# Performance work log

Measured on AMD Instinct MI355X. Metric: run time of the kernel, lower is better.

## Reference

```python
import jax, jax.numpy as jnp
import numpy as np

K = 10  # topk classes


def setup_inputs() -> dict:
    key = jax.random.key(0)
    ks = jax.random.split(key, 12)
    B, DF, M, C, V, DW, DT = 64, 768, 26, 3129, 10000, 300, 1024
    s = lambda k, sh, scale: jax.random.normal(k, sh, dtype=jnp.float32) * scale
    return {
        "ftm": s(ks[0], (B, DF, M, M), 1.0),
        "logits": s(ks[1], (B, C), 1.0),
        "labels": jax.random.randint(ks[2], (B,), 0, C, dtype=jnp.int32),
        "indices_table": jax.random.randint(ks[3], (C, 4), 0, V, dtype=jnp.int32),
        "word2vec": s(ks[4], (V, DW), 1.0),
        "W_emb": s(ks[5], (DW, DT), 1.0 / np.sqrt(DW)),
        "b_emb": jnp.zeros((DT,), jnp.float32),
        "W_cls": s(ks[6], (DT, DT), 1.0 / np.sqrt(DT)),
        "b_cls": jnp.zeros((DT,), jnp.float32),
        "W_v": s(ks[7], (DF, DT), 1.0 / np.sqrt(DF)),
        "b_v": jnp.zeros((DT,), jnp.float32),
        "W_bap": s(ks[8], (DT, DT), 1.0 / np.sqrt(DT)),
        "b_bap": jnp.zeros((DT,), jnp.float32),
        "W_fc": s(ks[9], (DT, K), 1.0 / np.sqrt(DT)),
        "b_fc": jnp.zeros((K,), jnp.float32),
    }


def reference(ftm, logits, labels, indices_table, word2vec,
              W_emb, b_emb, W_cls, b_cls, W_v, b_v, W_bap, b_bap, W_fc, b_fc):
    B, DF = ftm.shape[0], ftm.shape[1]
    C = logits.shape[1]
    # dispatch: topk classes, gather their word indices, embed
    _, topk_idx = jax.lax.top_k(logits, K)                  # [B, K]
    topk_cls = indices_table[topk_idx]                      # [B, K, 4]
    emb = word2vec[topk_cls].mean(axis=2)                   # [B, K, 300] (ClassEmbedding pooling)
    cls_emb = jax.nn.relu(emb @ W_emb + b_emb)              # [B, K, 1024]
    # SAC_BAP (dropouts in eval mode = identity)
    cls_emb = jax.nn.relu(cls_emb @ W_cls + b_cls)          # [B, K, 1024]
    f = ftm.reshape(B, DF, -1).transpose(0, 2, 1)           # [B, F, 768], F = m*m
    v = jax.nn.relu(f @ W_v + b_v)                          # [B, F, 1024]
    att_w_b_sfx = jnp.einsum('bfd,bkd->bfk', v, cls_emb)    # [B, F, K]
    att_w = jax.nn.softmax(att_w_b_sfx, axis=1)             # softmax over positions
    bap = jnp.einsum('bfd,bfk,bkd->bd', v, att_w, cls_emb)  # [B, 1024]
    bap = jax.nn.relu(bap @ W_bap + b_bap)                  # bap_emb_FC
    bap_logits = bap @ W_fc + b_fc                          # fc_new 1x1 conv -> [B, K]
    # combine: scatter topk logits into the full class space
    um = jnp.zeros((B, C), dtype=bap_logits.dtype)
    um = um.at[jnp.arange(B)[:, None], topk_idx].set(bap_logits)
    return um
```

## Files before the change

kernel.cpp:

```cpp
#include <hip/hip_runtime.h>
#include <hip/hip_bf16.h>

#define B_   64
#define C_   3129
#define K_   10
#define DF_  768
#define F_   676
#define DW_  300
#define DWP_ 320
#define DT_  1024
#define NSEG 4
#define FSEG 169

typedef __attribute__((ext_vector_type(8))) short short8;
typedef __attribute__((ext_vector_type(4))) float floatx4;

__device__ __forceinline__ void gload_lds16(const void* g, void* l) {
    __builtin_amdgcn_global_load_lds(
        (const __attribute__((address_space(1))) void*)g,
        (__attribute__((address_space(3))) void*)l, 16, 0, 0);
}

__global__ void topk_kernel(const float* __restrict__ logits,
                            int* __restrict__ topk_idx) {
    __shared__ float vals[C_];
    __shared__ float red_v[256];
    __shared__ int   red_i[256];
    int b = blockIdx.x;
    int tid = threadIdx.x;
    for (int i = tid; i < C_; i += 256) vals[i] = logits[(size_t)b * C_ + i];
    __syncthreads();
    for (int sel = 0; sel < K_; ++sel) {
        float bv = -INFINITY; int bi = 0x7fffffff;
        for (int i = tid; i < C_; i += 256) {
            float v = vals[i];
            if (v > bv) { bv = v; bi = i; }
        }
        red_v[tid] = bv; red_i[tid] = bi;
        __syncthreads();
        for (int s = 128; s > 0; s >>= 1) {
            if (tid < s) {
                float ov = red_v[tid + s]; int oi = red_i[tid + s];
                if (ov > red_v[tid] || (ov == red_v[tid] && oi < red_i[tid])) {
                    red_v[tid] = ov; red_i[tid] = oi;
                }
            }
            __syncthreads();
        }
        if (tid == 0) {
            topk_idx[b * K_ + sel] = red_i[0];
            vals[red_i[0]] = -INFINITY;
        }
        __syncthreads();
    }
}

__global__ void emb_kernel(const int* __restrict__ topk_idx,
                           const int* __restrict__ indices_table,
                           const float* __restrict__ word2vec,
                           __hip_bfloat16* __restrict__ emb) {
    int idx = blockIdx.x * blockDim.x + threadIdx.x;
    if (idx >= B_ * K_ * DWP_) return;
    int j  = idx % DWP_;
    int bk = idx / DWP_;
    float s = 0.f;
    if (j < DW_) {
        int cls = topk_idx[bk];
        const int* tbl = indices_table + (size_t)cls * 4;
        #pragma unroll
        for (int i = 0; i < 4; ++i) s += word2vec[(size_t)tbl[i] * DW_ + j];
        s *= 0.25f;
    }
    emb[idx] = (__hip_bfloat16)s;
}

__device__ __forceinline__ void tp_body(const float* __restrict__ s,
                                        __hip_bfloat16* __restrict__ d,
                                        int R, int Cc, int Rp, int c0, int r0) {
    __shared__ float tile[64][65];
    int t = threadIdx.x;
    int cl = (t & 15) * 4;
    int rl = t >> 4;
    #pragma unroll
    for (int i = 0; i < 4; ++i) {
        int r = rl + i * 16;
        float4 v = make_float4(0.f, 0.f, 0.f, 0.f);
        if (r0 + r < R && c0 + cl < Cc)
            v = *(const float4*)(s + (size_t)(r0 + r) * Cc + c0 + cl);
        tile[r][cl + 0] = v.x; tile[r][cl + 1] = v.y;
        tile[r][cl + 2] = v.z; tile[r][cl + 3] = v.w;
    }
    __syncthreads();
    int cw = t >> 2;
    int r4 = (t & 3) * 16;
    if (c0 + cw < Cc) {
        __align__(16) __hip_bfloat16 buf[16];
        #pragma unroll
        for (int j = 0; j < 16; ++j) buf[j] = (__hip_bfloat16)tile[r4 + j][cw];
        float4* dp = (float4*)(d + (size_t)(c0 + cw) * Rp + r0 + r4);
        dp[0] = *(float4*)&buf[0];
        dp[1] = *(float4*)&buf[8];
    }
}

__global__ __launch_bounds__(256)
void transpose_ftm(const float* __restrict__ src, __hip_bfloat16* __restrict__ dst) {
    tp_body(src + (size_t)blockIdx.z * DF_ * F_,
            dst + (size_t)blockIdx.z * F_ * DF_,
            DF_, F_, DF_, blockIdx.x * 64, blockIdx.y * 64);
}

__global__ __launch_bounds__(256)
void transpose_weights(const float* __restrict__ Wemb, __hip_bfloat16* __restrict__ WembT,
                       const float* __restrict__ Wcls, __hip_bfloat16* __restrict__ WclsT,
                       const float* __restrict__ Wv,   __hip_bfloat16* __restrict__ WvT,
                       const float* __restrict__ Wbap, __hip_bfloat16* __restrict__ WbapT) {
    int id = blockIdx.x;
    const float* s; __hip_bfloat16* d; int R, Rp;
    if (id < 80)       { s = Wemb; d = WembT; R = DW_;  Rp = DWP_; }
    else if (id < 336) { s = Wcls; d = WclsT; R = DT_;  Rp = DT_;  id -= 80;  }
    else if (id < 528) { s = Wv;   d = WvT;   R = DF_;  Rp = DF_;  id -= 336; }
    else               { s = Wbap; d = WbapT; R = DT_;  Rp = DT_;  id -= 528; }
    int bx = id & 15;
    int by = id >> 4;
    tp_body(s, d, R, DT_, Rp, bx * 64, by * 64);
}

template <int RELU, int OUTBF>
__global__ __launch_bounds__(256)
void gemm_mfma(const __hip_bfloat16* __restrict__ A,
               const __hip_bfloat16* __restrict__ Bt,
               const float* __restrict__ bias,
               void* __restrict__ Cout, int M, int N, int Kp) {
    __shared__ __align__(16) char smem[34816];
    __hip_bfloat16* As = (__hip_bfloat16*)smem;
    __hip_bfloat16* Bs = As + 128 * 64;
    int tid = threadIdx.x;
    int wave = tid >> 6, lane = tid & 63;
    int quad = lane >> 4, l16 = lane & 15;
    int wm = (wave & 1) * 64, wn = (wave >> 1) * 64;
    int n0 = blockIdx.x * 128;
    int m0 = blockIdx.y * 128;

    floatx4 acc[4][4];
    #pragma unroll
    for (int i = 0; i < 4; ++i)
        #pragma unroll
        for (int j = 0; j < 4; ++j)
            acc[i][j] = (floatx4){0.f, 0.f, 0.f, 0.f};

    int rsub = lane >> 3;
    int gchunk = (lane & 7) ^ rsub;

    int arow[4], brow[4];
    #pragma unroll
    for (int i = 0; i < 4; ++i) {
        arow[i] = wm + i * 16 + l16;
        brow[i] = wn + i * 16 + l16;
    }

    for (int k0 = 0; k0 < Kp; k0 += 64) {
        #pragma unroll
        for (int c = 0; c < 4; ++c) {
            int grp = wave * 4 + c;
            int row = grp * 8 + rsub;
            int ra = m0 + row; if (ra >= M) ra = M - 1;
            gload_lds16(A + (size_t)ra * Kp + k0 + gchunk * 8, As + grp * 512);
            gload_lds16(Bt + (size_t)(n0 + row) * Kp + k0 + gchunk * 8, Bs + grp * 512);
        }
        __syncthreads();
        #pragma unroll
        for (int ks = 0; ks < 2; ++ks) {
            short8 af[4], bf[4];
            #pragma unroll
            for (int mi = 0; mi < 4; ++mi)
                af[mi] = *(const short8*)&As[arow[mi] * 64 +
                            ((((ks << 2) | quad) ^ (arow[mi] & 7)) << 3)];
            #pragma unroll
            for (int ni = 0; ni < 4; ++ni)
                bf[ni] = *(const short8*)&Bs[brow[ni] * 64 +
                            ((((ks << 2) | quad) ^ (brow[ni] & 7)) << 3)];
            #pragma unroll
            for (int mi = 0; mi < 4; ++mi)
                #pragma unroll
                for (int ni = 0; ni < 4; ++ni)
                    acc[mi][ni] = __builtin_amdgcn_mfma_f32_16x16x32_bf16(
                        af[mi], bf[ni], acc[mi][ni], 0, 0, 0);
        }
        __syncthreads();
    }

    float bn[4];
    #pragma unroll
    for (int ni = 0; ni < 4; ++ni) bn[ni] = bias[n0 + wn + ni * 16 + l16];

    if (OUTBF) {
        __hip_bfloat16* Cs = (__hip_bfloat16*)smem;
        #pragma unroll
        for (int mi = 0; mi < 4; ++mi)
            #pragma unroll
            for (int rr = 0; rr < 4; ++rr) {
                int row = wm + mi * 16 + quad * 4 + rr;
                #pragma unroll
                for (int ni = 0; ni < 4; ++ni) {
                    float val = acc[mi][ni][rr] + bn[ni];
                    if (RELU) val = fmaxf(val, 0.f);
                    Cs[row * 136 + wn + ni * 16 + l16] = (__hip_bfloat16)val;
                }
            }
        __syncthreads();
        #pragma unroll
        for (int j = 0; j < 8; ++j) {
            int ch = tid + 256 * j;
            int row = ch >> 4, c16 = ch & 15;
            int r = m0 + row;
            float4 val = *(const float4*)&Cs[row * 136 + c16 * 8];
            if (r < M)
                *(float4*)((__hip_bfloat16*)Cout + (size_t)r * N + n0 + c16 * 8) = val;
        }
    } else {
        #pragma unroll
        for (int mi = 0; mi < 4; ++mi)
            #pragma unroll
            for (int rr = 0; rr < 4; ++rr) {
                int r = m0 + wm + mi * 16 + quad * 4 + rr;
                if (r < M) {
                    #pragma unroll
                    for (int ni = 0; ni < 4; ++ni) {
                        float val = acc[mi][ni][rr] + bn[ni];
                        if (RELU) val = fmaxf(val, 0.f);
                        ((float*)Cout)[(size_t)r * N + n0 + wn + ni * 16 + l16] = val;
                    }
                }
            }
    }
}

__global__ __launch_bounds__(256)
void attn_s_kernel(const __hip_bfloat16* __restrict__ v_buf,
                   const __hip_bfloat16* __restrict__ cls,
                   float* __restrict__ s_buf, int b0) {
    int tid = threadIdx.x;
    int wave = tid >> 6, lane = tid & 63;
    int bc = blockIdx.y;
    int f0 = blockIdx.x * 8 + wave * 2;
    int fa = f0 < F_ ? f0 : F_ - 1;
    int fb = (f0 + 1) < F_ ? f0 + 1 : F_ - 1;
    union U { float4 f4; __hip_bfloat16 h[8]; };
    const float4* va = (const float4*)(v_buf + ((size_t)(bc * F_ + fa)) * DT_ + lane * 16);
    const float4* vb = (const float4*)(v_buf + ((size_t)(bc * F_ + fb)) * DT_ + lane * 16);
    U a0, a1, b0u, b1u;
    a0.f4 = va[0]; a1.f4 = va[1];
    b0u.f4 = vb[0]; b1u.f4 = vb[1];
    float av[16], bv[16];
    #pragma unroll
    for (int i = 0; i < 8; ++i) {
        av[i] = (float)a0.h[i]; av[8 + i] = (float)a1.h[i];
        bv[i] = (float)b0u.h[i]; bv[8 + i] = (float)b1u.h[i];
    }
    const __hip_bfloat16* cp = cls + ((size_t)(b0 + bc) * K_) * DT_ + lane * 16;
    #pragma unroll
    for (int k = 0; k < K_; ++k) {
        const float4* c4 = (const float4*)(cp + (size_t)k * DT_);
        U c0u, c1u; c0u.f4 = c4[0]; c1u.f4 = c4[1];
        float da = 0.f, db = 0.f;
        #pragma unroll
        for (int i = 0; i < 8; ++i) {
            float cl0 = (float)c0u.h[i], cl1 = (float)c1u.h[i];
            da += av[i] * cl0 + av[8 + i] * cl1;
            db += bv[i] * cl0 + bv[8 + i] * cl1;
        }
        #pragma unroll
        for (int off = 32; off > 0; off >>= 1) {
            da += __shfl_down(da, off);
            db += __shfl_down(db, off);
        }
        if (lane == 0) {
            if (f0 < F_)     s_buf[((size_t)(bc * F_) + f0) * K_ + k] = da;
            if (f0 + 1 < F_) s_buf[((size_t)(bc * F_) + f0 + 1) * K_ + k] = db;
        }
    }
}

__global__ __launch_bounds__(64)
void softmax_stats(const float* __restrict__ s_buf, float2* __restrict__ ml,
                   int b0) {
    int k = blockIdx.x, bc = blockIdx.y, lane = threadIdx.x;
    const float* sp = s_buf + (size_t)bc * F_ * K_ + k;
    float m = -INFINITY;
    for (int f = lane; f < F_; f += 64) m = fmaxf(m, sp[(size_t)f * K_]);
    #pragma unroll
    for (int off = 32; off > 0; off >>= 1) m = fmaxf(m, __shfl_xor(m, off));
    float l = 0.f;
    for (int f = lane; f < F_; f += 64) l += __expf(sp[(size_t)f * K_] - m);
    #pragma unroll
    for (int off = 32; off > 0; off >>= 1) l += __shfl_xor(l, off);
    if (lane == 0) ml[(size_t)(b0 + bc) * K_ + k] = make_float2(m, 1.f / l);
}

__global__ __launch_bounds__(256)
void o_bap_partial(const __hip_bfloat16* __restrict__ v_buf,
                   const float* __restrict__ s_buf,
                   const float2* __restrict__ ml,
                   const __hip_bfloat16* __restrict__ cls,
                   float* __restrict__ pp, int b0) {
    int bc = blockIdx.x, seg = blockIdx.y;
    int b = b0 + bc;
    int t = threadIdx.x;
    int f0 = seg * FSEG;
    __shared__ float wbuf[FSEG * K_];
    __shared__ float mk[K_], rlk[K_];
    if (t < K_) {
        float2 v = ml[(size_t)b * K_ + t];
        mk[t] = v.x; rlk[t] = v.y;
    }
    __syncthreads();
    for (int j = t; j < FSEG * K_; j += 256) {
        int k = j % K_;
        float sv = s_buf[((size_t)bc * F_ + f0) * K_ + j];
        wbuf[j] = __expf(sv - mk[k]) * rlk[k];
    }
    __syncthreads();
    int d0 = t * 4;
    float acc[K_][4] = {};
    const __hip_bfloat16* vp = v_buf + ((size_t)bc * F_ + f0) * DT_ + d0;
    for (int f = 0; f < FSEG; ++f) {
        union { float2 f2; __hip_bfloat16 h[4]; } u;
        u.f2 = *(const float2*)(vp + (size_t)f * DT_);
        float vv[4];
        #pragma unroll
        for (int i = 0; i < 4; ++i) vv[i] = (float)u.h[i];
        const float* wk = &wbuf[f * K_];
        #pragma unroll
        for (int k = 0; k < K_; ++k)
            #pragma unroll
            for (int i = 0; i < 4; ++i) acc[k][i] += wk[k] * vv[i];
    }
    union { float2 f2; __hip_bfloat16 h[4]; } cu;
    float outv[4] = {};
    #pragma unroll
    for (int k = 0; k < K_; ++k) {
        cu.f2 = *(const float2*)(cls + ((size_t)b * K_ + k) * DT_ + d0);
        #pragma unroll
        for (int i = 0; i < 4; ++i) outv[i] += acc[k][i] * (float)cu.h[i];
    }
    float* pd = pp + ((size_t)seg * B_ + b) * DT_ + d0;
    *(float4*)pd = *(float4*)outv;
}

__global__ void bap_combine(const float* __restrict__ pp,
                            __hip_bfloat16* __restrict__ bap) {
    int idx = blockIdx.x * 256 + threadIdx.x;
    float s = pp[idx] + pp[idx + B_ * DT_] + pp[idx + 2 * B_ * DT_]
            + pp[idx + 3 * B_ * DT_];
    bap[idx] = (__hip_bfloat16)s;
}

__global__ void final_kernel(const float* __restrict__ y,
                             const float* __restrict__ Wfc,
                             const float* __restrict__ bfc,
                             const int* __restrict__ topk_idx,
                             float* __restrict__ out) {
    int b = blockIdx.x, tid = threadIdx.x;
    int lane = tid & 63, wave = tid >> 6;
    float pk[K_] = {};
    for (int d = tid; d < DT_; d += 256) {
        float yv = y[(size_t)b * DT_ + d];
        #pragma unroll
        for (int k = 0; k < K_; ++k) pk[k] += yv * Wfc[(size_t)d * K_ + k];
    }
    __shared__ float wsum[4][K_];
    #pragma unroll
    for (int k = 0; k < K_; ++k) {
        float a = pk[k];
        #pragma unroll
        for (int off = 32; off > 0; off >>= 1) a += __shfl_down(a, off);
        if (lane == 0) wsum[wave][k] = a;
    }
    __syncthreads();
    if (tid < K_) {
        float lg = wsum[0][tid] + wsum[1][tid] + wsum[2][tid] + wsum[3][tid] + bfc[tid];
        out[(size_t)b * C_ + topk_idx[b * K_ + tid]] = lg;
    }
}

extern "C" void kernel_launch(void* const* d_in, const int* in_sizes, int n_in,
                              void* d_out, int out_size, void* d_ws, size_t ws_size,
                              hipStream_t stream) {
    const float* ftm           = (const float*)d_in[0];
    const float* logits        = (const float*)d_in[1];
    const int*   indices_table = (const int*)d_in[3];
    const float* word2vec      = (const float*)d_in[4];
    const float* W_emb         = (const float*)d_in[5];
    const float* b_emb         = (const float*)d_in[6];
    const float* W_cls         = (const float*)d_in[7];
    const float* b_cls         = (const float*)d_in[8];
    const float* W_v           = (const float*)d_in[9];
    const float* b_v           = (const float*)d_in[10];
    const float* W_bap         = (const float*)d_in[11];
    const float* b_bap         = (const float*)d_in[12];
    const float* W_fc          = (const float*)d_in[13];
    const float* b_fc          = (const float*)d_in[14];
    float* out = (float*)d_out;

    char* ws = (char*)d_ws;
    size_t off = 0;
    auto alloc = [&](size_t bytes) -> void* {
        void* p = ws + off;
        off = (off + bytes + 255) & ~(size_t)255;
        return p;
    };
    int*            topk_idx = (int*)           alloc((size_t)B_ * K_ * 4);
    __hip_bfloat16* emb_bf   = (__hip_bfloat16*)alloc((size_t)B_ * K_ * DWP_ * 2);
    __hip_bfloat16* cls1     = (__hip_bfloat16*)alloc((size_t)B_ * K_ * DT_ * 2);
    __hip_bfloat16* cls2     = (__hip_bfloat16*)alloc((size_t)B_ * K_ * DT_ * 2);
    __hip_bfloat16* Wemb_t   = (__hip_bfloat16*)alloc((size_t)DT_ * DWP_ * 2);
    __hip_bfloat16* Wcls_t   = (__hip_bfloat16*)alloc((size_t)DT_ * DT_ * 2);
    __hip_bfloat16* Wv_t     = (__hip_bfloat16*)alloc((size_t)DT_ * DF_ * 2);
    __hip_bfloat16* Wbap_t   = (__hip_bfloat16*)alloc((size_t)DT_ * DT_ * 2);
    float*          s_buf    = (float*)         alloc((size_t)B_ * F_ * K_ * 4);
    float2*         ml       = (float2*)        alloc((size_t)B_ * K_ * 8);
    float*          pp       = (float*)         alloc((size_t)NSEG * B_ * DT_ * 4);
    __hip_bfloat16* bap_bf   = (__hip_bfloat16*)alloc((size_t)B_ * DT_ * 2);
    float*          yb       = (float*)         alloc((size_t)B_ * DT_ * 4);

    size_t per_b = (size_t)F_ * DF_ * 2 + (size_t)F_ * DT_ * 2;
    size_t avail = (ws_size > off + 8192) ? ws_size - off - 8192 : 0;
    int nb = (int)(avail / per_b);
    if (nb > B_) nb = B_;
    if (nb < 1) nb = 1;
    __hip_bfloat16* ftm_t = (__hip_bfloat16*)alloc((size_t)nb * F_ * DF_ * 2);
    __hip_bfloat16* v_buf = (__hip_bfloat16*)alloc((size_t)nb * F_ * DT_ * 2);

    hipMemsetAsync(d_out, 0, (size_t)out_size * sizeof(float), stream);

    topk_kernel<<<B_, 256, 0, stream>>>(logits, topk_idx);
    emb_kernel<<<(B_ * K_ * DWP_ + 255) / 256, 256, 0, stream>>>(
        topk_idx, indices_table, word2vec, emb_bf);

    transpose_weights<<<784, 256, 0, stream>>>(
        W_emb, Wemb_t, W_cls, Wcls_t, W_v, Wv_t, W_bap, Wbap_t);

    gemm_mfma<1, 1><<<dim3(DT_ / 128, (B_ * K_ + 127) / 128), 256, 0, stream>>>(
        emb_bf, Wemb_t, b_emb, cls1, B_ * K_, DT_, DWP_);
    gemm_mfma<1, 1><<<dim3(DT_ / 128, (B_ * K_ + 127) / 128), 256, 0, stream>>>(
        cls1, Wcls_t, b_cls, cls2, B_ * K_, DT_, DT_);

    for (int b0 = 0; b0 < B_; b0 += nb) {
        int cb = min(nb, B_ - b0);
        transpose_ftm<<<dim3((F_ + 63) / 64, DF_ / 64, cb), 256, 0, stream>>>(
            ftm + (size_t)b0 * DF_ * F_, ftm_t);
        int M = cb * F_;
        gemm_mfma<1, 1><<<dim3(DT_ / 128, (M + 127) / 128), 256, 0, stream>>>(
            ftm_t, Wv_t, b_v, v_buf, M, DT_, DF_);
        float* s_c = s_buf + (size_t)b0 * F_ * K_;
        attn_s_kernel<<<dim3((F_ + 7) / 8, cb), 256, 0, stream>>>(
            v_buf, cls2, s_c, b0);
        softmax_stats<<<dim3(K_, cb), 64, 0, stream>>>(s_c, ml, b0);
        o_bap_partial<<<dim3(cb, NSEG), 256, 0, stream>>>(
            v_buf, s_c, ml, cls2, pp, b0);
    }
    bap_combine<<<B_ * DT_ / 256, 256, 0, stream>>>(pp, bap_bf);

    gemm_mfma<1, 0><<<dim3(DT_ / 128, 1), 256, 0, stream>>>(
        bap_bf, Wbap_t, b_bap, yb, B_, DT_, DT_);
    final_kernel<<<B_, 256, 0, stream>>>(yb, W_fc, b_fc, topk_idx, out);
}
```

Baseline: 533.8 us.

## Split o_bap across more position segments, widen loads, and remap GEMM tiles per XCD

Raises the number of position segments in the attention-weighted reduction from 4 to 13, giving more blocks per batch. Inside each block the two halves of the threads split the segment's positions, use 8-wide bf16 loads, and combine their results through shared memory. The GEMM remaps its flat block id so that consecutive tiles land on the same XCD, aiming for better L2 reuse. The cost is more partial sums for bap_combine to read and more registers per thread for the wider accumulators.

```diff
diff --git a/kernel.cpp b/kernel.cpp
--- a/kernel.cpp
+++ b/kernel.cpp
@@ -9,8 +9,8 @@
 #define DW_  300
 #define DWP_ 320
 #define DT_  1024
-#define NSEG 4
-#define FSEG 169
+#define NSEG 13
+#define FSEG 52
 
 typedef __attribute__((ext_vector_type(8))) short short8;
 typedef __attribute__((ext_vector_type(4))) float floatx4;
@@ -139,8 +139,15 @@
     int wave = tid >> 6, lane = tid & 63;
     int quad = lane >> 4, l16 = lane & 15;
     int wm = (wave & 1) * 64, wn = (wave >> 1) * 64;
-    int n0 = blockIdx.x * 128;
-    int m0 = blockIdx.y * 128;
+
+    int gx = gridDim.x;
+    int nwg = gx * gridDim.y;
+    int flat = blockIdx.y * gx + blockIdx.x;
+    int q = nwg >> 3, r = nwg & 7;
+    int xcd = flat & 7, lid = flat >> 3;
+    int o = (xcd < r ? xcd * (q + 1) : r * (q + 1) + (xcd - r) * q) + lid;
+    int n0 = (o % gx) * 128;
+    int m0 = (o / gx) * 128;
 
     floatx4 acc[4][4];
     #pragma unroll
@@ -310,6 +317,7 @@
     int f0 = seg * FSEG;
     __shared__ float wbuf[FSEG * K_];
     __shared__ float mk[K_], rlk[K_];
+    __shared__ float red[128 * 8];
     if (t < K_) {
         float2 v = ml[(size_t)b * K_ + t];
         mk[t] = v.x; rlk[t] = v.y;
@@ -321,38 +329,51 @@
         wbuf[j] = __expf(sv - mk[k]) * rlk[k];
     }
     __syncthreads();
-    int d0 = t * 4;
-    float acc[K_][4] = {};
-    const __hip_bfloat16* vp = v_buf + ((size_t)bc * F_ + f0) * DT_ + d0;
-    for (int f = 0; f < FSEG; ++f) {
-        union { float2 f2; __hip_bfloat16 h[4]; } u;
-        u.f2 = *(const float2*)(vp + (size_t)f * DT_);
-        float vv[4];
-        #pragma unroll
-        for (int i = 0; i < 4; ++i) vv[i] = (float)u.h[i];
-        const float* wk = &wbuf[f * K_];
+    int th = t & 127, half = t >> 7;
+    int d0 = th * 8;
+    int fs = half * (FSEG / 2);
+    float acc[K_][8] = {};
+    const __hip_bfloat16* vp = v_buf + ((size_t)bc * F_ + f0 + fs) * DT_ + d0;
+    for (int f = 0; f < FSEG / 2; ++f) {
+        union { float4 f4; __hip_bfloat16 h[8]; } u;
+        u.f4 = *(const float4*)(vp + (size_t)f * DT_);
+        float vv[8];
+        #pragma unroll
+        for (int i = 0; i < 8; ++i) vv[i] = (float)u.h[i];
+        const float* wk = &wbuf[(fs + f) * K_];
         #pragma unroll
         for (int k = 0; k < K_; ++k)
             #pragma unroll
-            for (int i = 0; i < 4; ++i) acc[k][i] += wk[k] * vv[i];
-    }
-    union { float2 f2; __hip_bfloat16 h[4]; } cu;
-    float outv[4] = {};
+            for (int i = 0; i < 8; ++i) acc[k][i] += wk[k] * vv[i];
+    }
+    float outv[8] = {};
+    union { float4 f4; __hip_bfloat16 h[8]; } cu;
     #pragma unroll
     for (int k = 0; k < K_; ++k) {
-        cu.f2 = *(const float2*)(cls + ((size_t)b * K_ + k) * DT_ + d0);
-        #pragma unroll
-        for (int i = 0; i < 4; ++i) outv[i] += acc[k][i] * (float)cu.h[i];
-    }
-    float* pd = pp + ((size_t)seg * B_ + b) * DT_ + d0;
-    *(float4*)pd = *(float4*)outv;
+        cu.f4 = *(const float4*)(cls + ((size_t)b * K_ + k) * DT_ + d0);
+        #pragma unroll
+        for (int i = 0; i < 8; ++i) outv[i] += acc[k][i] * (float)cu.h[i];
+    }
+    if (half == 1) {
+        *(float4*)&red[th * 8]     = *(float4*)&outv[0];
+        *(float4*)&red[th * 8 + 4] = *(float4*)&outv[4];
+    }
+    __syncthreads();
+    if (half == 0) {
+        #pragma unroll
+        for (int i = 0; i < 8; ++i) outv[i] += red[th * 8 + i];
+        float* pd = pp + ((size_t)seg * B_ + b) * DT_ + d0;
+        *(float4*)pd       = *(float4*)&outv[0];
+        *(float4*)(pd + 4) = *(float4*)&outv[4];
+    }
 }
 
 __global__ void bap_combine(const float* __restrict__ pp,
                             __hip_bfloat16* __restrict__ bap) {
     int idx = blockIdx.x * 256 + threadIdx.x;
-    float s = pp[idx] + pp[idx + B_ * DT_] + pp[idx + 2 * B_ * DT_]
-            + pp[idx + 3 * B_ * DT_];
+    float s = 0.f;
+    #pragma unroll
+    for (int g = 0; g < NSEG; ++g) s += pp[idx + (size_t)g * B_ * DT_];
     bap[idx] = (__hip_bfloat16)s;
 }
 
```

Result: faster. 479.7 us (-10.1%).
